# Performance work log

Measured on AMD Instinct MI355X. Metric: run time of the kernel, lower is better.

## Reference

```python
import jax, jax.numpy as jnp
import numpy as np


def log_g(x):
    # log of the 'continuous' g: g(x) = x + 0.5 for x>=0, sigmoid(x) otherwise
    return jnp.where(x >= 0, jnp.log(jax.nn.relu(x) + 0.5), -jax.nn.softplus(-x))


def setup_inputs() -> dict:
    key = jax.random.key(0)
    ks = jax.random.split(key, 6)
    B, T, D, H = 8, 4096, 1024, 1024
    s = 1.0 / np.sqrt(D)
    return {
        "x": jax.random.normal(ks[0], (B, T, D), dtype=jnp.float32),
        "h_0": jax.random.uniform(ks[1], (B, 1, H), dtype=jnp.float32),
        "Wz": jax.random.normal(ks[2], (D, H), dtype=jnp.float32) * s,
        "bz": jnp.zeros((H,), dtype=jnp.float32),
        "Wh": jax.random.normal(ks[3], (D, H), dtype=jnp.float32) * s,
        "bh": jnp.zeros((H,), dtype=jnp.float32),
    }


def reference(x, h_0, Wz, bz, Wh, bh):
    # x: [B,T,D], h_0: [B,1,H]
    k = jnp.einsum('btd,dh->bth', x, Wz) + bz            # gate pre-activation
    log_z = -jax.nn.softplus(-k)                          # log sigmoid(k)
    log_coeffs = -jax.nn.softplus(k)                      # log (1 - sigmoid(k))
    log_h0 = log_g(h_0)                                   # [B,1,H]
    log_tilde_h = log_g(jnp.einsum('btd,dh->bth', x, Wh) + bh)
    # parallel scan in log space over time axis
    a_star = jnp.pad(jnp.cumsum(log_coeffs, axis=1), ((0, 0), (1, 0), (0, 0)))  # [B,T+1,H]
    log_values = jnp.concatenate([log_h0, log_z + log_tilde_h], axis=1)          # [B,T+1,H]
    log_h = a_star + jax.lax.cumlogsumexp(log_values - a_star, axis=1)
    return jnp.exp(log_h)  # [B,T+1,H]
```

## Files before the change

### kernel.cpp

```cpp
#include <hip/hip_runtime.h>
#include <hip/hip_bf16.h>
#include <cstdint>
#include <cstddef>

#define B_ 8
#define T_ 4096
#define D_ 1024
#define H_ 1024
#define M_ (B_*T_)
#define NCHUNK 64
#define CLEN 64

using bf16x8   = __attribute__((ext_vector_type(8))) __bf16;
using floatx4  = __attribute__((ext_vector_type(4))) float;
using float4v  = __attribute__((ext_vector_type(4))) float;
using ushort4v = __attribute__((ext_vector_type(4))) unsigned short;
using aw2_t    = __attribute__((ext_vector_type(2))) _Float16;
using halfx8   = __attribute__((ext_vector_type(8))) _Float16;

__device__ inline unsigned short f2bf(float f) {
  union { float f; unsigned u; } v; v.f = f;
  unsigned u = v.u;
  u += 0x7fffu + ((u >> 16) & 1u);
  return (unsigned short)(u >> 16);
}

__device__ inline void async_load16(const void* g, void* l) {
  __builtin_amdgcn_global_load_lds((const __attribute__((address_space(1))) void*)g,
                                   (__attribute__((address_space(3))) void*)l,
                                   16, 0, 0);
}

__global__ __launch_bounds__(256) void cast_x_kernel(const float* __restrict__ x,
                                                     unsigned short* __restrict__ xb) {
  size_t i = (size_t)blockIdx.x * 256 + threadIdx.x;
  float4v v = ((const float4v*)x)[i];
  ushort4v o = { f2bf(v[0]), f2bf(v[1]), f2bf(v[2]), f2bf(v[3]) };
  ((ushort4v*)xb)[i] = o;
}

__global__ __launch_bounds__(256) void transpose_w_kernel(const float* __restrict__ Wz,
                                                          const float* __restrict__ Wh,
                                                          unsigned short* __restrict__ Wzt,
                                                          unsigned short* __restrict__ Wht) {
  __shared__ float tile[32][33];
  const float* W = blockIdx.z ? Wh : Wz;
  unsigned short* Wt = blockIdx.z ? Wht : Wzt;
  int n0 = blockIdx.x * 32, k0 = blockIdx.y * 32;
#pragma unroll
  for (int j = 0; j < 4; ++j) {
    int kr = threadIdx.y + j * 8;
    tile[kr][threadIdx.x] = W[(size_t)(k0 + kr) * H_ + n0 + threadIdx.x];
  }
  __syncthreads();
#pragma unroll
  for (int j = 0; j < 4; ++j) {
    int nr = threadIdx.y + j * 8;
    Wt[(size_t)(n0 + nr) * D_ + k0 + threadIdx.x] = f2bf(tile[threadIdx.x][nr]);
  }
}

__global__ __launch_bounds__(256) void gemm_kernel(
    const unsigned short* __restrict__ xb,
    const unsigned short* __restrict__ wzt,
    const unsigned short* __restrict__ wht,
    const float* __restrict__ bz, const float* __restrict__ bh,
    aw2_t* __restrict__ aw_out) {
  __shared__ __align__(16) unsigned short ldsA[128 * 32];
  __shared__ __align__(16) unsigned short ldsBz[64 * 32];
  __shared__ __align__(16) unsigned short ldsBh[64 * 32];

  const int tid = threadIdx.x;
  const int lane = tid & 63, wid = tid >> 6;
  const int wm = wid >> 1, wn = wid & 1;
  const int row16 = lane & 15, quad = lane >> 4;
  const int m0 = blockIdx.y * 128, n0 = blockIdx.x * 64;

  floatx4 accz[4][2], acch[4][2];
#pragma unroll
  for (int mi = 0; mi < 4; ++mi)
#pragma unroll
    for (int ni = 0; ni < 2; ++ni) {
      accz[mi][ni] = (floatx4){0.f, 0.f, 0.f, 0.f};
      acch[mi][ni] = (floatx4){0.f, 0.f, 0.f, 0.f};
    }

  for (int kk = 0; kk < D_; kk += 32) {
    {
      int s = tid;
      async_load16(xb + (size_t)(m0 + (s >> 2)) * D_ + kk + (s & 3) * 8, &ldsA[s * 8]);
      s = tid + 256;
      async_load16(xb + (size_t)(m0 + (s >> 2)) * D_ + kk + (s & 3) * 8, &ldsA[s * 8]);
      s = tid;
      async_load16(wzt + (size_t)(n0 + (s >> 2)) * D_ + kk + (s & 3) * 8, &ldsBz[s * 8]);
      async_load16(wht + (size_t)(n0 + (s >> 2)) * D_ + kk + (s & 3) * 8, &ldsBh[s * 8]);
    }
    __syncthreads();

    bf16x8 af[4], bzf[2], bhf[2];
#pragma unroll
    for (int mi = 0; mi < 4; ++mi)
      af[mi] = *(const bf16x8*)&ldsA[(wm * 64 + mi * 16 + row16) * 32 + quad * 8];
#pragma unroll
    for (int ni = 0; ni < 2; ++ni) {
      bzf[ni] = *(const bf16x8*)&ldsBz[(wn * 32 + ni * 16 + row16) * 32 + quad * 8];
      bhf[ni] = *(const bf16x8*)&ldsBh[(wn * 32 + ni * 16 + row16) * 32 + quad * 8];
    }
#pragma unroll
    for (int mi = 0; mi < 4; ++mi)
#pragma unroll
      for (int ni = 0; ni < 2; ++ni) {
        accz[mi][ni] = __builtin_amdgcn_mfma_f32_16x16x32_bf16(af[mi], bzf[ni], accz[mi][ni], 0, 0, 0);
        acch[mi][ni] = __builtin_amdgcn_mfma_f32_16x16x32_bf16(af[mi], bhf[ni], acch[mi][ni], 0, 0, 0);
      }
    __syncthreads();
  }

#pragma unroll
  for (int mi = 0; mi < 4; ++mi) {
#pragma unroll
    for (int ni = 0; ni < 2; ++ni) {
      int col = n0 + wn * 32 + ni * 16 + row16;
      float bzv = bz[col], bhv = bh[col];
#pragma unroll
      for (int r = 0; r < 4; ++r) {
        int row = m0 + wm * 64 + mi * 16 + quad * 4 + r;
        float k   = accz[mi][ni][r] + bzv;
        float pre = acch[mi][ni][r] + bhv;
        float z  = 1.f / (1.f + __expf(-k));
        float av = 1.f / (1.f + __expf(k));
        float g  = (pre >= 0.f) ? (pre + 0.5f) : 1.f / (1.f + __expf(-pre));
        aw2_t o = { (_Float16)av, (_Float16)(z * g) };
        aw_out[(size_t)row * H_ + col] = o;
      }
    }
  }
}

__global__ __launch_bounds__(256) void scan_pass1(const halfx8* __restrict__ aw,
                                                  float* __restrict__ P, float* __restrict__ S) {
  int c = blockIdx.x;
  int b = blockIdx.y;
  int h4 = threadIdx.x;
  size_t base = (size_t)(b * T_ + c * CLEN) * (H_ / 4) + h4;
  float p0 = 1.f, p1 = 1.f, p2 = 1.f, p3 = 1.f;
  float s0 = 0.f, s1 = 0.f, s2 = 0.f, s3 = 0.f;
#pragma unroll 8
  for (int i = 0; i < CLEN; ++i) {
    halfx8 v = aw[base + (size_t)i * (H_ / 4)];
    float a0 = (float)v[0], w0 = (float)v[1];
    float a1 = (float)v[2], w1 = (float)v[3];
    float a2 = (float)v[4], w2 = (float)v[5];
    float a3 = (float)v[6], w3 = (float)v[7];
    s0 = a0 * s0 + w0; p0 *= a0;
    s1 = a1 * s1 + w1; p1 *= a1;
    s2 = a2 * s2 + w2; p2 *= a2;
    s3 = a3 * s3 + w3; p3 *= a3;
  }
  size_t o = ((size_t)b * H_ + h4 * 4) * NCHUNK + c;
  P[o] = p0; P[o + NCHUNK] = p1; P[o + 2 * NCHUNK] = p2; P[o + 3 * NCHUNK] = p3;
  S[o] = s0; S[o + NCHUNK] = s1; S[o + 2 * NCHUNK] = s2; S[o + 3 * NCHUNK] = s3;
}

__global__ __launch_bounds__(256) void scan_pass2(const float* __restrict__ h0,
                                                  const float* __restrict__ P,
                                                  const float* __restrict__ S,
                                                  float* __restrict__ carry,
                                                  float* __restrict__ out) {
  int gid = blockIdx.x * 256 + threadIdx.x;
  int b = gid >> 10, h = gid & 1023;
  float v = h0[(size_t)b * H_ + h];
  float cur = (v >= 0.f) ? (v + 0.5f) : 1.f / (1.f + __expf(-v));
  out[((size_t)b * (T_ + 1)) * H_ + h] = cur;
  const float4v* Pv = (const float4v*)&P[((size_t)b * H_ + h) * NCHUNK];
  const float4v* Sv = (const float4v*)&S[((size_t)b * H_ + h) * NCHUNK];
  float4v* Cv = (float4v*)&carry[((size_t)b * H_ + h) * NCHUNK];
#pragma unroll
  for (int j = 0; j < NCHUNK / 4; ++j) {
    float4v p = Pv[j], s = Sv[j], cc;
    cc[0] = cur; cur = p[0] * cur + s[0];
    cc[1] = cur; cur = p[1] * cur + s[1];
    cc[2] = cur; cur = p[2] * cur + s[2];
    cc[3] = cur; cur = p[3] * cur + s[3];
    Cv[j] = cc;
  }
}

__global__ __launch_bounds__(256) void scan_pass3(const halfx8* __restrict__ aw,
                                                  const float* __restrict__ carry,
                                                  float* __restrict__ out) {
  int c = blockIdx.x;
  int b = blockIdx.y;
  int h4 = threadIdx.x;
  size_t base = (size_t)(b * T_ + c * CLEN) * (H_ / 4) + h4;
  size_t cb = ((size_t)b * H_ + h4 * 4) * NCHUNK + c;
  float c0 = carry[cb], c1 = carry[cb + NCHUNK], c2 = carry[cb + 2 * NCHUNK], c3 = carry[cb + 3 * NCHUNK];
  size_t obase = ((size_t)b * (T_ + 1) + c * CLEN + 1) * (H_ / 4) + h4;
  float4v* outv = (float4v*)out;
#pragma unroll 8
  for (int i = 0; i < CLEN; ++i) {
    halfx8 v = aw[base + (size_t)i * (H_ / 4)];
    c0 = (float)v[0] * c0 + (float)v[1];
    c1 = (float)v[2] * c1 + (float)v[3];
    c2 = (float)v[4] * c2 + (float)v[5];
    c3 = (float)v[6] * c3 + (float)v[7];
    float4v o = { c0, c1, c2, c3 };
    outv[obase + (size_t)i * (H_ / 4)] = o;
  }
}

extern "C" void kernel_launch(void* const* d_in, const int* in_sizes, int n_in,
                              void* d_out, int out_size, void* d_ws, size_t ws_size,
                              hipStream_t stream) {
  const float* x  = (const float*)d_in[0];
  const float* h0 = (const float*)d_in[1];
  const float* Wz = (const float*)d_in[2];
  const float* bz = (const float*)d_in[3];
  const float* Wh = (const float*)d_in[4];
  const float* bh = (const float*)d_in[5];
  float* out = (float*)d_out;

  char* ws = (char*)d_ws;
  unsigned short* xb  = (unsigned short*)(ws);
  unsigned short* wzt = (unsigned short*)(ws + 67108864ULL);
  unsigned short* wht = (unsigned short*)(ws + 69206016ULL);
  aw2_t* aw_ws = (aw2_t*)(ws + 71303168ULL);
  float* P_ws  = (float*)(ws + 71303168ULL + 134217728ULL);
  float* S_ws  = (float*)(ws + 71303168ULL + 134217728ULL + 2097152ULL);
  float* c_ws  = (float*)(ws + 71303168ULL + 134217728ULL + 2ULL * 2097152ULL);

  hipLaunchKernelGGL(cast_x_kernel, dim3(32768), dim3(256), 0, stream, x, xb);
  hipLaunchKernelGGL(transpose_w_kernel, dim3(32, 32, 2), dim3(32, 8), 0, stream, Wz, Wh, wzt, wht);
  hipLaunchKernelGGL(gemm_kernel, dim3(16, 256), dim3(256), 0, stream,
                     xb, wzt, wht, bz, bh, aw_ws);
  hipLaunchKernelGGL(scan_pass1, dim3(NCHUNK, B_), dim3(256), 0, stream,
                     (const halfx8*)aw_ws, P_ws, S_ws);
  hipLaunchKernelGGL(scan_pass2, dim3(32), dim3(256), 0, stream, h0, P_ws, S_ws, c_ws, out);
  hipLaunchKernelGGL(scan_pass3, dim3(NCHUNK, B_), dim3(256), 0, stream,
                     (const halfx8*)aw_ws, c_ws, out);
}
```

Before: 504.2 us.

## Load GEMM weight fragments directly from global, remap blocks per XCD, widen cast

The GEMM stops staging the Wz/Wh tiles in LDS. Each lane now reads its bf16x8 B fragments straight from global memory into registers, and only the x tile still goes through async LDS copies. The grid is flattened and remapped so that blocks landing on the same XCD (g&7) share M rows, aiming for better L2 reuse of the x tile. The cast kernel now handles two float4 per thread with half the blocks. Direct global B loads remove LDS traffic but put weight-load latency in front of the MFMAs with no prefetch, and can depend on L2 hit rates.

```diff
diff --git a/kernel.cpp b/kernel.cpp
--- a/kernel.cpp
+++ b/kernel.cpp
@@ -33,10 +33,13 @@
 
 __global__ __launch_bounds__(256) void cast_x_kernel(const float* __restrict__ x,
                                                      unsigned short* __restrict__ xb) {
-  size_t i = (size_t)blockIdx.x * 256 + threadIdx.x;
-  float4v v = ((const float4v*)x)[i];
-  ushort4v o = { f2bf(v[0]), f2bf(v[1]), f2bf(v[2]), f2bf(v[3]) };
-  ((ushort4v*)xb)[i] = o;
+  size_t i = ((size_t)blockIdx.x * 256 + threadIdx.x) * 2;
+#pragma unroll
+  for (int j = 0; j < 2; ++j) {
+    float4v v = ((const float4v*)x)[i + j];
+    ushort4v o = { f2bf(v[0]), f2bf(v[1]), f2bf(v[2]), f2bf(v[3]) };
+    ((ushort4v*)xb)[i + j] = o;
+  }
 }
 
 __global__ __launch_bounds__(256) void transpose_w_kernel(const float* __restrict__ Wz,
@@ -67,14 +70,17 @@
     const float* __restrict__ bz, const float* __restrict__ bh,
     aw2_t* __restrict__ aw_out) {
   __shared__ __align__(16) unsigned short ldsA[128 * 32];
-  __shared__ __align__(16) unsigned short ldsBz[64 * 32];
-  __shared__ __align__(16) unsigned short ldsBh[64 * 32];
 
   const int tid = threadIdx.x;
   const int lane = tid & 63, wid = tid >> 6;
   const int wm = wid >> 1, wn = wid & 1;
   const int row16 = lane & 15, quad = lane >> 4;
-  const int m0 = blockIdx.y * 128, n0 = blockIdx.x * 64;
+
+  int g = blockIdx.x;
+  int x = g & 7, j = g >> 3;
+  int n_idx = j & 15;
+  int m_idx = (x << 5) | (j >> 4);
+  const int m0 = m_idx * 128, n0 = n_idx * 64;
 
   floatx4 accz[4][2], acch[4][2];
 #pragma unroll
@@ -85,27 +91,32 @@
       acch[mi][ni] = (floatx4){0.f, 0.f, 0.f, 0.f};
     }
 
+  const char* bzp[2];
+  const char* bhp[2];
+#pragma unroll
+  for (int ni = 0; ni < 2; ++ni) {
+    int row = n0 + wn * 32 + ni * 16 + row16;
+    bzp[ni] = (const char*)(wzt + (size_t)row * D_ + quad * 8);
+    bhp[ni] = (const char*)(wht + (size_t)row * D_ + quad * 8);
+  }
+  const unsigned short* arow0 = xb + (size_t)(m0 + (tid >> 2)) * D_ + (tid & 3) * 8;
+  const unsigned short* arow1 = xb + (size_t)(m0 + 64 + (tid >> 2)) * D_ + (tid & 3) * 8;
+
   for (int kk = 0; kk < D_; kk += 32) {
-    {
-      int s = tid;
-      async_load16(xb + (size_t)(m0 + (s >> 2)) * D_ + kk + (s & 3) * 8, &ldsA[s * 8]);
-      s = tid + 256;
-      async_load16(xb + (size_t)(m0 + (s >> 2)) * D_ + kk + (s & 3) * 8, &ldsA[s * 8]);
-      s = tid;
-      async_load16(wzt + (size_t)(n0 + (s >> 2)) * D_ + kk + (s & 3) * 8, &ldsBz[s * 8]);
-      async_load16(wht + (size_t)(n0 + (s >> 2)) * D_ + kk + (s & 3) * 8, &ldsBh[s * 8]);
+    async_load16(arow0 + kk, &ldsA[tid * 8]);
+    async_load16(arow1 + kk, &ldsA[(tid + 256) * 8]);
+    bf16x8 bzf[2], bhf[2];
+#pragma unroll
+    for (int ni = 0; ni < 2; ++ni) {
+      bzf[ni] = *(const bf16x8*)(bzp[ni] + kk * 2);
+      bhf[ni] = *(const bf16x8*)(bhp[ni] + kk * 2);
     }
     __syncthreads();
 
-    bf16x8 af[4], bzf[2], bhf[2];
+    bf16x8 af[4];
 #pragma unroll
     for (int mi = 0; mi < 4; ++mi)
       af[mi] = *(const bf16x8*)&ldsA[(wm * 64 + mi * 16 + row16) * 32 + quad * 8];
-#pragma unroll
-    for (int ni = 0; ni < 2; ++ni) {
-      bzf[ni] = *(const bf16x8*)&ldsBz[(wn * 32 + ni * 16 + row16) * 32 + quad * 8];
-      bhf[ni] = *(const bf16x8*)&ldsBh[(wn * 32 + ni * 16 + row16) * 32 + quad * 8];
-    }
 #pragma unroll
     for (int mi = 0; mi < 4; ++mi)
 #pragma unroll
@@ -129,8 +140,8 @@
         float pre = acch[mi][ni][r] + bhv;
         float z  = 1.f / (1.f + __expf(-k));
         float av = 1.f / (1.f + __expf(k));
-        float g  = (pre >= 0.f) ? (pre + 0.5f) : 1.f / (1.f + __expf(-pre));
-        aw2_t o = { (_Float16)av, (_Float16)(z * g) };
+        float gg = (pre >= 0.f) ? (pre + 0.5f) : 1.f / (1.f + __expf(-pre));
+        aw2_t o = { (_Float16)av, (_Float16)(z * gg) };
         aw_out[(size_t)row * H_ + col] = o;
       }
     }
@@ -229,9 +240,9 @@
   float* S_ws  = (float*)(ws + 71303168ULL + 134217728ULL + 2097152ULL);
   float* c_ws  = (float*)(ws + 71303168ULL + 134217728ULL + 2ULL * 2097152ULL);
 
-  hipLaunchKernelGGL(cast_x_kernel, dim3(32768), dim3(256), 0, stream, x, xb);
+  hipLaunchKernelGGL(cast_x_kernel, dim3(16384), dim3(256), 0, stream, x, xb);
   hipLaunchKernelGGL(transpose_w_kernel, dim3(32, 32, 2), dim3(32, 8), 0, stream, Wz, Wh, wzt, wht);
-  hipLaunchKernelGGL(gemm_kernel, dim3(16, 256), dim3(256), 0, stream,
+  hipLaunchKernelGGL(gemm_kernel, dim3(4096), dim3(256), 0, stream,
                      xb, wzt, wht, bz, bh, aw_ws);
   hipLaunchKernelGGL(scan_pass1, dim3(NCHUNK, B_), dim3(256), 0, stream,
                      (const halfx8*)aw_ws, P_ws, S_ws);
```

After: 620.9 us. 23.2% more time.
